# Optimization experiments

Measured on AMD Instinct MI355X. Metric: run time of the kernel, lower is better.

The kernel has to match this reference:

```python
import jax, jax.numpy as jnp
import numpy as np

N = 100000   # vertices
M = 20000    # hyperedges
NNZ = 1000000  # incidence pairs
L = 50000    # candidate links
K = 2        # vertices per link
IN, H, OUT = 256, 256, 128


def setup_inputs() -> dict:
    key = jax.random.key(0)
    ks = jax.random.split(key, 8)
    X = jax.random.normal(ks[0], (N, IN), jnp.float32)
    v_idx = jax.random.randint(ks[1], (NNZ,), 0, N, jnp.int32)
    e_idx = jax.random.randint(ks[2], (NNZ,), 0, M, jnp.int32)
    link = jax.random.randint(ks[3], (L, K), 0, N, jnp.int32)
    init = lambda k, sh, fan: jax.random.normal(k, sh, jnp.float32) / np.float32(np.sqrt(fan))
    W1 = init(ks[4], (IN, H), IN)
    b1 = jnp.zeros((H,), jnp.float32)
    W2 = init(ks[5], (H, OUT), H)
    b2 = jnp.zeros((OUT,), jnp.float32)
    fc_w = init(ks[6], (OUT, 1), OUT)
    fc_b = jnp.zeros((1,), jnp.float32)
    return dict(X=X, W1=W1, b1=b1, W2=W2, b2=b2, fc_w=fc_w, fc_b=fc_b,
                v_idx=v_idx, e_idx=e_idx, link=link)


def _segment_mean(vals, idx, num_segments):
    # mean aggregation: segment sum / segment count (count clamped to 1)
    s = jax.ops.segment_sum(vals, idx, num_segments=num_segments)
    c = jax.ops.segment_sum(jnp.ones((idx.shape[0], 1), vals.dtype), idx,
                            num_segments=num_segments)
    return s / jnp.maximum(c, 1.0)


def _hgnn_conv(X, W, b, v_idx, e_idx):
    # theta -> v2e mean -> e2v mean -> ReLU (dropout = identity in eval)
    Xt = X @ W + b                              # [N, d_out]
    Y = _segment_mean(Xt[v_idx], e_idx, M)      # [M, d_out] hyperedge feats
    Xv = _segment_mean(Y[e_idx], v_idx, N)      # [N, d_out] back to vertices
    return jax.nn.relu(Xv)


def reference(X, W1, b1, W2, b2, fc_w, fc_b, v_idx, e_idx, link):
    h1 = _hgnn_conv(X, W1, b1, v_idx, e_idx)    # extra .relu() in encode is idempotent
    h2 = _hgnn_conv(h1, W2, b2, v_idx, e_idx)   # [N, OUT]
    # per-link mean of member vertex embeddings (vectorized gather-mean)
    ex = h2[link].mean(axis=1)                  # [L, OUT]
    return jax.nn.sigmoid(ex @ fc_w + fc_b)     # [L, 1]
```

## Files before the change

kernel.cpp:

```cpp
#include <hip/hip_runtime.h>
#include <cstdint>
#include <cstddef>

#define IN_DIM  256
#define H_DIM   256
#define OUT_DIM 128
#define MEDGES  20000

typedef unsigned short u16;
typedef unsigned int   u32;
typedef short bf16x8 __attribute__((ext_vector_type(8)));
typedef float f32x4  __attribute__((ext_vector_type(4)));

__device__ __forceinline__ float bf2f(u16 u) {
    u32 x = ((u32)u) << 16;
    float f;
    __builtin_memcpy(&f, &x, 4);
    return f;
}
__device__ __forceinline__ u16 f2bf(float f) {
    u32 x;
    __builtin_memcpy(&x, &f, 4);
    u32 r = x + 0x7fffu + ((x >> 16) & 1u);
    return (u16)(r >> 16);
}

__global__ void cvt_all(const float4* __restrict__ X,  ushort4* __restrict__ Xb,  int nX,
                        const float4* __restrict__ W1, ushort4* __restrict__ W1b, int nW1,
                        const float4* __restrict__ W2, ushort4* __restrict__ W2b, int nW2)
{
    int i = blockIdx.x * blockDim.x + threadIdx.x;
    const float4* s; ushort4* d; int k;
    if (i < nX)                  { s = X;  d = Xb;  k = i; }
    else if (i < nX + nW1)       { s = W1; d = W1b; k = i - nX; }
    else if (i < nX + nW1 + nW2) { s = W2; d = W2b; k = i - nX - nW1; }
    else return;
    float4 v = s[k];
    ushort4 o;
    o.x = f2bf(v.x); o.y = f2bf(v.y); o.z = f2bf(v.z); o.w = f2bf(v.w);
    d[k] = o;
}

__global__ void hist_rank_split(const int* __restrict__ e_idx, const int* __restrict__ v_idx,
                                int* __restrict__ cnt_e, int* __restrict__ cnt_v,
                                int* __restrict__ rank_e, int* __restrict__ rank_v, int nnz)
{
    int i = blockIdx.x * blockDim.x + threadIdx.x;
    if (i < nnz) {
        rank_e[i] = atomicAdd(&cnt_e[e_idx[i]], 1);
    } else if (i < 2 * nnz) {
        int j = i - nnz;
        rank_v[j] = atomicAdd(&cnt_v[v_idx[j]], 1);
    }
}

#define SCAN_B 1024
__global__ void scan_block_both(const int* __restrict__ cnt_e, int* __restrict__ e_off,
                                const int* __restrict__ cnt_v, int* __restrict__ v_off,
                                int* __restrict__ bsums, int m, int n, int nbE)
{
    __shared__ int s[SCAN_B];
    const int* in; int* out; int* bs; int nn; int blk;
    if ((int)blockIdx.x < nbE) { in = cnt_e; out = e_off; bs = bsums;      nn = m; blk = blockIdx.x; }
    else                       { in = cnt_v; out = v_off; bs = bsums + 64; nn = n; blk = blockIdx.x - nbE; }
    int gid = blk * SCAN_B + threadIdx.x;
    int x = (gid < nn) ? in[gid] : 0;
    s[threadIdx.x] = x;
    __syncthreads();
    for (int off = 1; off < SCAN_B; off <<= 1) {
        int v = (threadIdx.x >= off) ? s[threadIdx.x - off] : 0;
        __syncthreads();
        s[threadIdx.x] += v;
        __syncthreads();
    }
    if (gid < nn) out[gid] = s[threadIdx.x] - x;
    if (threadIdx.x == SCAN_B - 1) bs[blk] = s[SCAN_B - 1];
}

__global__ void scan_top_both(int* __restrict__ bsums, int nbE, int nbV,
                              int* __restrict__ e_off, int* __restrict__ v_off,
                              int m, int n, int nnz)
{
    int t = threadIdx.x;
    if (t == 0) {
        int run = 0;
        for (int i = 0; i < nbE; ++i) { int v = bsums[i]; bsums[i] = run; run += v; }
        e_off[m] = nnz;
    } else if (t == 1) {
        int run = 0;
        for (int i = 0; i < nbV; ++i) { int v = bsums[64 + i]; bsums[64 + i] = run; run += v; }
        v_off[n] = nnz;
    }
}

__global__ void scan_add_both(int* __restrict__ e_off, int* __restrict__ v_off,
                              const int* __restrict__ bsums, int m, int n, int nbE)
{
    int* out; const int* bs; int nn; int blk;
    if ((int)blockIdx.x < nbE) { out = e_off; bs = bsums;      nn = m; blk = blockIdx.x; }
    else                       { out = v_off; bs = bsums + 64; nn = n; blk = blockIdx.x - nbE; }
    int gid = blk * SCAN_B + threadIdx.x;
    if (gid < nn) out[gid] += bs[blk];
}

__global__ void scatter_split(const int* __restrict__ e_idx, const int* __restrict__ v_idx,
                              const int* __restrict__ e_off, const int* __restrict__ v_off,
                              const int* __restrict__ rank_e, const int* __restrict__ rank_v,
                              int* __restrict__ e_list, int* __restrict__ v_list, int nnz)
{
    int i = blockIdx.x * blockDim.x + threadIdx.x;
    if (i < nnz) {
        int e = e_idx[i];
        e_list[e_off[e] + rank_e[i]] = v_idx[i];
    } else if (i < 2 * nnz) {
        int j = i - nnz;
        int v = v_idx[j];
        v_list[v_off[v] + rank_v[j]] = e_idx[j];
    }
}

__global__ void seg_mean_w4(const ushort4* __restrict__ src, ushort4* __restrict__ dst,
                            const int* __restrict__ off, const int* __restrict__ lst,
                            int nseg, int do_relu)
{
    int wid  = (blockIdx.x * blockDim.x + threadIdx.x) >> 6;
    int lane = threadIdx.x & 63;
    if (wid >= nseg) return;
    int beg = __builtin_amdgcn_readfirstlane(off[wid]);
    int end = __builtin_amdgcn_readfirstlane(off[wid + 1]);
    float ax = 0.f, ay = 0.f, az = 0.f, aw = 0.f;
    int j = beg;
    for (; j + 3 < end; j += 4) {
        int i0 = lst[j], i1 = lst[j + 1], i2 = lst[j + 2], i3 = lst[j + 3];
        ushort4 a = src[(size_t)i0 * 64 + lane];
        ushort4 b = src[(size_t)i1 * 64 + lane];
        ushort4 c = src[(size_t)i2 * 64 + lane];
        ushort4 d = src[(size_t)i3 * 64 + lane];
        ax += bf2f(a.x) + bf2f(b.x) + bf2f(c.x) + bf2f(d.x);
        ay += bf2f(a.y) + bf2f(b.y) + bf2f(c.y) + bf2f(d.y);
        az += bf2f(a.z) + bf2f(b.z) + bf2f(c.z) + bf2f(d.z);
        aw += bf2f(a.w) + bf2f(b.w) + bf2f(c.w) + bf2f(d.w);
    }
    for (; j < end; ++j) {
        ushort4 a = src[(size_t)lst[j] * 64 + lane];
        ax += bf2f(a.x); ay += bf2f(a.y); az += bf2f(a.z); aw += bf2f(a.w);
    }
    int cnt = end - beg;
    float inv = (cnt > 0) ? 1.f / (float)cnt : 0.f;
    ax *= inv; ay *= inv; az *= inv; aw *= inv;
    if (do_relu) {
        ax = fmaxf(ax, 0.f); ay = fmaxf(ay, 0.f);
        az = fmaxf(az, 0.f); aw = fmaxf(aw, 0.f);
    }
    ushort4 o;
    o.x = f2bf(ax); o.y = f2bf(ay); o.z = f2bf(az); o.w = f2bf(aw);
    dst[(size_t)wid * 64 + lane] = o;
}

__global__ void seg_mean_w2(const ushort2* __restrict__ src, ushort2* __restrict__ dst,
                            const int* __restrict__ off, const int* __restrict__ lst,
                            int nseg, int do_relu)
{
    int wid  = (blockIdx.x * blockDim.x + threadIdx.x) >> 6;
    int lane = threadIdx.x & 63;
    if (wid >= nseg) return;
    int beg = __builtin_amdgcn_readfirstlane(off[wid]);
    int end = __builtin_amdgcn_readfirstlane(off[wid + 1]);
    float ax = 0.f, ay = 0.f;
    int j = beg;
    for (; j + 3 < end; j += 4) {
        int i0 = lst[j], i1 = lst[j + 1], i2 = lst[j + 2], i3 = lst[j + 3];
        ushort2 a = src[(size_t)i0 * 64 + lane];
        ushort2 b = src[(size_t)i1 * 64 + lane];
        ushort2 c = src[(size_t)i2 * 64 + lane];
        ushort2 d = src[(size_t)i3 * 64 + lane];
        ax += bf2f(a.x) + bf2f(b.x) + bf2f(c.x) + bf2f(d.x);
        ay += bf2f(a.y) + bf2f(b.y) + bf2f(c.y) + bf2f(d.y);
    }
    for (; j < end; ++j) {
        ushort2 a = src[(size_t)lst[j] * 64 + lane];
        ax += bf2f(a.x); ay += bf2f(a.y);
    }
    int cnt = end - beg;
    float inv = (cnt > 0) ? 1.f / (float)cnt : 0.f;
    ax *= inv; ay *= inv;
    if (do_relu) { ax = fmaxf(ax, 0.f); ay = fmaxf(ay, 0.f); }
    ushort2 o;
    o.x = f2bf(ax); o.y = f2bf(ay);
    dst[(size_t)wid * 64 + lane] = o;
}

#define GSTRIDE 40
__global__ __launch_bounds__(256) void gemm_mfma_bf16(const u16* __restrict__ A,
                                                      const u16* __restrict__ W,
                                                      const float* __restrict__ bias,
                                                      u16* __restrict__ C,
                                                      int R, int K, int Cc)
{
    __shared__ __align__(16) u16 As[64 * GSTRIDE];
    __shared__ __align__(16) u16 Bs[64 * GSTRIDE];

    int tid  = threadIdx.x;
    int wave = tid >> 6;
    int lane = tid & 63;
    int quad = lane >> 4;
    int l16  = lane & 15;

    int row0 = blockIdx.y * 64;
    int col0 = blockIdx.x * 64;

    f32x4 acc[4] = {};

    int ar   = tid >> 2;
    int aseg = tid & 3;
    int bk   = tid >> 3;
    int bn   = tid & 7;

    for (int k0 = 0; k0 < K; k0 += 32) {
        bf16x8 av = {};
        int gr = row0 + ar;
        if (gr < R) av = *(const bf16x8*)&A[(size_t)gr * K + k0 + 8 * aseg];
        *(bf16x8*)&As[ar * GSTRIDE + 8 * aseg] = av;
        bf16x8 wv = *(const bf16x8*)&W[(size_t)(k0 + bk) * Cc + col0 + 8 * bn];
#pragma unroll
        for (int j = 0; j < 8; ++j)
            Bs[(8 * bn + j) * GSTRIDE + bk] = ((const u16*)&wv)[j];
        __syncthreads();

        bf16x8 af = *(const bf16x8*)&As[(16 * wave + l16) * GSTRIDE + 8 * quad];
#pragma unroll
        for (int nt = 0; nt < 4; ++nt) {
            bf16x8 bfv = *(const bf16x8*)&Bs[(16 * nt + l16) * GSTRIDE + 8 * quad];
            acc[nt] = __builtin_amdgcn_mfma_f32_16x16x32_bf16(af, bfv, acc[nt], 0, 0, 0);
        }
        __syncthreads();
    }

#pragma unroll
    for (int nt = 0; nt < 4; ++nt) {
        int col = col0 + 16 * nt + l16;
        float bv = bias[col];
#pragma unroll
        for (int r = 0; r < 4; ++r) {
            int grow = row0 + 16 * wave + 4 * quad + r;
            if (grow < R) C[(size_t)grow * Cc + col] = f2bf(acc[nt][r] + bv);
        }
    }
}

__global__ void link_head(const ushort2* __restrict__ h2, const int* __restrict__ link,
                          const float* __restrict__ fc_w, const float* __restrict__ fc_b,
                          float* __restrict__ out, int L)
{
    int gtid = blockIdx.x * blockDim.x + threadIdx.x;
    int wid  = gtid >> 6;
    int lane = threadIdx.x & 63;
    if (wid >= L) return;
    const int Dh = OUT_DIM / 2;
    int a = link[2 * wid + 0];
    int b = link[2 * wid + 1];
    ushort2 ra = h2[(size_t)a * Dh + lane];
    ushort2 rb = h2[(size_t)b * Dh + lane];
    float2 w = *(const float2*)&fc_w[2 * lane];
    float acc = 0.5f * ((bf2f(ra.x) + bf2f(rb.x)) * w.x + (bf2f(ra.y) + bf2f(rb.y)) * w.y);
#pragma unroll
    for (int off = 32; off; off >>= 1) acc += __shfl_xor(acc, off, 64);
    if (lane == 0) out[wid] = 1.f / (1.f + expf(-(acc + fc_b[0])));
}


static inline size_t align_up(size_t x, size_t a) { return (x + a - 1) & ~(a - 1); }

extern "C" void kernel_launch(void* const* d_in, const int* in_sizes, int n_in,
                              void* d_out, int out_size, void* d_ws, size_t ws_size,
                              hipStream_t stream)
{
    const float* X   = (const float*)d_in[0];
    const float* W1  = (const float*)d_in[1];
    const float* b1  = (const float*)d_in[2];
    const float* W2  = (const float*)d_in[3];
    const float* b2  = (const float*)d_in[4];
    const float* fcw = (const float*)d_in[5];
    const float* fcb = (const float*)d_in[6];
    const int* v_idx = (const int*)d_in[7];
    const int* e_idx = (const int*)d_in[8];
    const int* link  = (const int*)d_in[9];
    float* out = (float*)d_out;

    const int NNZ = in_sizes[7];
    const int N   = in_sizes[0] / IN_DIM;
    const int L   = in_sizes[9] / 2;
    const int M   = MEDGES;
    const int Mpad = (int)align_up(M, 64);

    char* p = (char*)d_ws;
    auto carve = [&](size_t bytes) -> void* {
        void* r = (void*)p;
        p += align_up(bytes, 256);
        return r;
    };
    u16*  Xb    = (u16*)carve((size_t)N * IN_DIM * 2);
    u16*  h1b   = (u16*)carve((size_t)N * H_DIM * 2);
    u16*  Aggb  = (u16*)carve((size_t)M * H_DIM * 2);
    u16*  Yb    = (u16*)carve((size_t)M * H_DIM * 2);
    u16*  W1b   = (u16*)carve((size_t)IN_DIM * H_DIM * 2);
    u16*  W2b   = (u16*)carve((size_t)H_DIM * OUT_DIM * 2);
    int*  e_off = (int*)carve((size_t)(M + 1) * 4);
    int*  v_off = (int*)carve((size_t)(N + 1) * 4);
    int*  cnt_e = (int*)carve((size_t)(Mpad + N) * 4);
    int*  cnt_v = cnt_e + Mpad;
    int*  rank_e= (int*)carve((size_t)NNZ * 4);
    int*  rank_v= (int*)carve((size_t)NNZ * 4);
    int*  e_lst = (int*)carve((size_t)NNZ * 4);
    int*  v_lst = (int*)carve((size_t)NNZ * 4);
    int*  bsums = (int*)carve(1024);

    (void)hipMemsetAsync(cnt_e, 0, (size_t)(Mpad + N) * 4, stream);

    const int tb = 256;

    int nX  = N * IN_DIM / 4;
    int nW1 = IN_DIM * H_DIM / 4;
    int nW2 = H_DIM * OUT_DIM / 4;
    cvt_all<<<(nX + nW1 + nW2 + tb - 1) / tb, tb, 0, stream>>>(
        (const float4*)X, (ushort4*)Xb, nX,
        (const float4*)W1, (ushort4*)W1b, nW1,
        (const float4*)W2, (ushort4*)W2b, nW2);

    hist_rank_split<<<(2 * NNZ + tb - 1) / tb, tb, 0, stream>>>(e_idx, v_idx, cnt_e, cnt_v,
                                                                rank_e, rank_v, NNZ);

    int nbE = (M + SCAN_B - 1) / SCAN_B;
    int nbV = (N + SCAN_B - 1) / SCAN_B;
    scan_block_both<<<nbE + nbV, SCAN_B, 0, stream>>>(cnt_e, e_off, cnt_v, v_off, bsums, M, N, nbE);
    scan_top_both<<<1, 64, 0, stream>>>(bsums, nbE, nbV, e_off, v_off, M, N, NNZ);
    scan_add_both<<<nbE + nbV, SCAN_B, 0, stream>>>(e_off, v_off, bsums, M, N, nbE);

    scatter_split<<<(2 * NNZ + tb - 1) / tb, tb, 0, stream>>>(e_idx, v_idx, e_off, v_off,
                                                              rank_e, rank_v, e_lst, v_lst, NNZ);

    seg_mean_w4<<<((size_t)M * 64 + tb - 1) / tb, tb, 0, stream>>>(
        (const ushort4*)Xb, (ushort4*)Aggb, e_off, e_lst, M, 0);
    gemm_mfma_bf16<<<dim3(H_DIM / 64, (M + 63) / 64), 256, 0, stream>>>(Aggb, W1b, b1, Yb, M, IN_DIM, H_DIM);
    seg_mean_w4<<<((size_t)N * 64 + tb - 1) / tb, tb, 0, stream>>>(
        (const ushort4*)Yb, (ushort4*)h1b, v_off, v_lst, N, 1);

    seg_mean_w4<<<((size_t)M * 64 + tb - 1) / tb, tb, 0, stream>>>(
        (const ushort4*)h1b, (ushort4*)Aggb, e_off, e_lst, M, 0);
    gemm_mfma_bf16<<<dim3(OUT_DIM / 64, (M + 63) / 64), 256, 0, stream>>>(Aggb, W2b, b2, Yb, M, H_DIM, OUT_DIM);
    seg_mean_w2<<<((size_t)N * 64 + tb - 1) / tb, tb, 0, stream>>>(
        (const ushort2*)Yb, (ushort2*)Xb, v_off, v_lst, N, 1);

    link_head<<<((size_t)L * 64 + tb - 1) / tb, tb, 0, stream>>>(
        (const ushort2*)Xb, link, fcw, fcb, out, L);
}
```

Before: 577.5 us.

## Replicate histogram counters per XCD to reduce cross-die atomic contention

The CSR-building histogram now keeps a separate counter array for each of the eight XCDs, chosen by reading the hardware XCC id, so atomics stay inside a die's local L2. Each rank is tagged in its top bits with the replica it came from. The scan sums the replicas and writes a per-replica exclusive base, and the scatter uses that base to place each entry. The cost is an 8x larger memset and more scan traffic, and the counter arrays borrow the h1b buffer as scratch space.

```diff
diff --git a/kernel.cpp b/kernel.cpp
--- a/kernel.cpp
+++ b/kernel.cpp
@@ -23,6 +23,12 @@
     __builtin_memcpy(&x, &f, 4);
     u32 r = x + 0x7fffu + ((x >> 16) & 1u);
     return (u16)(r >> 16);
+}
+
+__device__ __forceinline__ int xcc_id() {
+    int x;
+    asm volatile("s_getreg_b32 %0, hwreg(HW_REG_XCC_ID)" : "=s"(x));
+    return x & 7;
 }
 
 __global__ void cvt_all(const float4* __restrict__ X,  ushort4* __restrict__ Xb,  int nX,
@@ -41,30 +47,42 @@
     d[k] = o;
 }
 
-__global__ void hist_rank_split(const int* __restrict__ e_idx, const int* __restrict__ v_idx,
-                                int* __restrict__ cnt_e, int* __restrict__ cnt_v,
-                                int* __restrict__ rank_e, int* __restrict__ rank_v, int nnz)
-{
+__global__ void hist_rank_xcd(const int* __restrict__ e_idx, const int* __restrict__ v_idx,
+                              int* __restrict__ cnt_rep,
+                              u32* __restrict__ rank_e, u32* __restrict__ rank_v,
+                              int nnz, int seg, int mpad)
+{
+    int r = xcc_id();
+    int* my = cnt_rep + (size_t)r * seg;
+    u32 tag = (u32)r << 28;
     int i = blockIdx.x * blockDim.x + threadIdx.x;
     if (i < nnz) {
-        rank_e[i] = atomicAdd(&cnt_e[e_idx[i]], 1);
+        u32 old = (u32)atomicAdd(&my[e_idx[i]], 1);
+        rank_e[i] = old | tag;
     } else if (i < 2 * nnz) {
         int j = i - nnz;
-        rank_v[j] = atomicAdd(&cnt_v[v_idx[j]], 1);
+        u32 old = (u32)atomicAdd(&my[mpad + v_idx[j]], 1);
+        rank_v[j] = old | tag;
     }
 }
 
 #define SCAN_B 1024
-__global__ void scan_block_both(const int* __restrict__ cnt_e, int* __restrict__ e_off,
-                                const int* __restrict__ cnt_v, int* __restrict__ v_off,
-                                int* __restrict__ bsums, int m, int n, int nbE)
+__global__ void scan_block_both(int* __restrict__ cnt_rep,
+                                int* __restrict__ e_off, int* __restrict__ v_off,
+                                int* __restrict__ bsums, int m, int n, int nbE,
+                                int seg, int mpad)
 {
     __shared__ int s[SCAN_B];
-    const int* in; int* out; int* bs; int nn; int blk;
-    if ((int)blockIdx.x < nbE) { in = cnt_e; out = e_off; bs = bsums;      nn = m; blk = blockIdx.x; }
-    else                       { in = cnt_v; out = v_off; bs = bsums + 64; nn = n; blk = blockIdx.x - nbE; }
+    int* out; int* bs; int nn; int blk; int boff;
+    if ((int)blockIdx.x < nbE) { out = e_off; bs = bsums;      nn = m; blk = blockIdx.x;       boff = 0; }
+    else                       { out = v_off; bs = bsums + 64; nn = n; blk = blockIdx.x - nbE; boff = mpad; }
     int gid = blk * SCAN_B + threadIdx.x;
-    int x = (gid < nn) ? in[gid] : 0;
+    int c[8];
+    int x = 0;
+    if (gid < nn) {
+#pragma unroll
+        for (int r = 0; r < 8; ++r) { c[r] = cnt_rep[(size_t)r * seg + boff + gid]; x += c[r]; }
+    }
     s[threadIdx.x] = x;
     __syncthreads();
     for (int off = 1; off < SCAN_B; off <<= 1) {
@@ -73,7 +91,17 @@
         s[threadIdx.x] += v;
         __syncthreads();
     }
-    if (gid < nn) out[gid] = s[threadIdx.x] - x;
+    if (gid < nn) {
+        int ex = s[threadIdx.x] - x;
+        out[gid] = ex;
+        int run = ex;
+#pragma unroll
+        for (int r = 0; r < 8; ++r) {
+            int cc = c[r];
+            cnt_rep[(size_t)r * seg + boff + gid] = run;
+            run += cc;
+        }
+    }
     if (threadIdx.x == SCAN_B - 1) bs[blk] = s[SCAN_B - 1];
 }
 
@@ -94,28 +122,39 @@
 }
 
 __global__ void scan_add_both(int* __restrict__ e_off, int* __restrict__ v_off,
-                              const int* __restrict__ bsums, int m, int n, int nbE)
-{
-    int* out; const int* bs; int nn; int blk;
-    if ((int)blockIdx.x < nbE) { out = e_off; bs = bsums;      nn = m; blk = blockIdx.x; }
-    else                       { out = v_off; bs = bsums + 64; nn = n; blk = blockIdx.x - nbE; }
+                              int* __restrict__ cnt_rep, const int* __restrict__ bsums,
+                              int m, int n, int nbE, int seg, int mpad)
+{
+    int* out; const int* bs; int nn; int blk; int boff;
+    if ((int)blockIdx.x < nbE) { out = e_off; bs = bsums;      nn = m; blk = blockIdx.x;       boff = 0; }
+    else                       { out = v_off; bs = bsums + 64; nn = n; blk = blockIdx.x - nbE; boff = mpad; }
     int gid = blk * SCAN_B + threadIdx.x;
-    if (gid < nn) out[gid] += bs[blk];
+    if (gid < nn) {
+        int add = bs[blk];
+        out[gid] += add;
+#pragma unroll
+        for (int r = 0; r < 8; ++r) cnt_rep[(size_t)r * seg + boff + gid] += add;
+    }
 }
 
 __global__ void scatter_split(const int* __restrict__ e_idx, const int* __restrict__ v_idx,
-                              const int* __restrict__ e_off, const int* __restrict__ v_off,
-                              const int* __restrict__ rank_e, const int* __restrict__ rank_v,
-                              int* __restrict__ e_list, int* __restrict__ v_list, int nnz)
+                              const int* __restrict__ cnt_rep,
+                              const u32* __restrict__ rank_e, const u32* __restrict__ rank_v,
+                              int* __restrict__ e_list, int* __restrict__ v_list,
+                              int nnz, int seg, int mpad)
 {
     int i = blockIdx.x * blockDim.x + threadIdx.x;
     if (i < nnz) {
+        u32 pr = rank_e[i];
+        int r = (int)(pr >> 28);
         int e = e_idx[i];
-        e_list[e_off[e] + rank_e[i]] = v_idx[i];
+        e_list[cnt_rep[(size_t)r * seg + e] + (int)(pr & 0x0FFFFFFFu)] = v_idx[i];
     } else if (i < 2 * nnz) {
         int j = i - nnz;
+        u32 pr = rank_v[j];
+        int r = (int)(pr >> 28);
         int v = v_idx[j];
-        v_list[v_off[v] + rank_v[j]] = e_idx[j];
+        v_list[cnt_rep[(size_t)r * seg + mpad + v] + (int)(pr & 0x0FFFFFFFu)] = e_idx[j];
     }
 }
 
@@ -292,6 +331,7 @@
     const int L   = in_sizes[9] / 2;
     const int M   = MEDGES;
     const int Mpad = (int)align_up(M, 64);
+    const int SEG  = Mpad + N;
 
     char* p = (char*)d_ws;
     auto carve = [&](size_t bytes) -> void* {
@@ -307,15 +347,15 @@
     u16*  W2b   = (u16*)carve((size_t)H_DIM * OUT_DIM * 2);
     int*  e_off = (int*)carve((size_t)(M + 1) * 4);
     int*  v_off = (int*)carve((size_t)(N + 1) * 4);
-    int*  cnt_e = (int*)carve((size_t)(Mpad + N) * 4);
-    int*  cnt_v = cnt_e + Mpad;
     int*  rank_e= (int*)carve((size_t)NNZ * 4);
     int*  rank_v= (int*)carve((size_t)NNZ * 4);
     int*  e_lst = (int*)carve((size_t)NNZ * 4);
     int*  v_lst = (int*)carve((size_t)NNZ * 4);
     int*  bsums = (int*)carve(1024);
 
-    (void)hipMemsetAsync(cnt_e, 0, (size_t)(Mpad + N) * 4, stream);
+    int* cnt_rep = (int*)h1b;
+
+    (void)hipMemsetAsync(cnt_rep, 0, (size_t)8 * SEG * 4, stream);
 
     const int tb = 256;
 
@@ -327,17 +367,17 @@
         (const float4*)W1, (ushort4*)W1b, nW1,
         (const float4*)W2, (ushort4*)W2b, nW2);
 
-    hist_rank_split<<<(2 * NNZ + tb - 1) / tb, tb, 0, stream>>>(e_idx, v_idx, cnt_e, cnt_v,
-                                                                rank_e, rank_v, NNZ);
+    hist_rank_xcd<<<(2 * NNZ + tb - 1) / tb, tb, 0, stream>>>(
+        e_idx, v_idx, cnt_rep, (u32*)rank_e, (u32*)rank_v, NNZ, SEG, Mpad);
 
     int nbE = (M + SCAN_B - 1) / SCAN_B;
     int nbV = (N + SCAN_B - 1) / SCAN_B;
-    scan_block_both<<<nbE + nbV, SCAN_B, 0, stream>>>(cnt_e, e_off, cnt_v, v_off, bsums, M, N, nbE);
+    scan_block_both<<<nbE + nbV, SCAN_B, 0, stream>>>(cnt_rep, e_off, v_off, bsums, M, N, nbE, SEG, Mpad);
     scan_top_both<<<1, 64, 0, stream>>>(bsums, nbE, nbV, e_off, v_off, M, N, NNZ);
-    scan_add_both<<<nbE + nbV, SCAN_B, 0, stream>>>(e_off, v_off, bsums, M, N, nbE);
-
-    scatter_split<<<(2 * NNZ + tb - 1) / tb, tb, 0, stream>>>(e_idx, v_idx, e_off, v_off,
-                                                              rank_e, rank_v, e_lst, v_lst, NNZ);
+    scan_add_both<<<nbE + nbV, SCAN_B, 0, stream>>>(e_off, v_off, cnt_rep, bsums, M, N, nbE, SEG, Mpad);
+
+    scatter_split<<<(2 * NNZ + tb - 1) / tb, tb, 0, stream>>>(
+        e_idx, v_idx, cnt_rep, (const u32*)rank_e, (const u32*)rank_v, e_lst, v_lst, NNZ, SEG, Mpad);
 
     seg_mean_w4<<<((size_t)M * 64 + tb - 1) / tb, tb, 0, stream>>>(
         (const ushort4*)Xb, (ushort4*)Aggb, e_off, e_lst, M, 0);
```

Measured after the change: 574.9 us. About the same (-0.4%).

## Replace global-atomic CSR build with per-block LDS histograms and local scatter

Applied to the files above, without the earlier changes.

Builds the CSR incidence lists with per-block shared-memory histograms packed as 16-bit counters, instead of global atomics and stored per-element rank arrays. A column-wise prefix over per-block count rows gives each block its base offsets, and the scatter pass reuses LDS atomics to assign slots. This removes the global atomic contention, the memset and the two NNZ-sized rank arrays. In exchange it adds a strided per-column pass over 384 count rows in the scan kernel, and the vertex path makes four passes over its index chunk. The count matrices reuse the h1b buffer as scratch.

```diff
diff --git a/kernel.cpp b/kernel.cpp
--- a/kernel.cpp
+++ b/kernel.cpp
@@ -6,6 +6,12 @@
 #define H_DIM   256
 #define OUT_DIM 128
 #define MEDGES  20000
+
+#define B_E 256
+#define B_V 128
+#define QN  25600
+#define QW  (QN / 2)
+#define CT  1024
 
 typedef unsigned short u16;
 typedef unsigned int   u32;
@@ -41,30 +47,72 @@
     d[k] = o;
 }
 
-__global__ void hist_rank_split(const int* __restrict__ e_idx, const int* __restrict__ v_idx,
-                                int* __restrict__ cnt_e, int* __restrict__ cnt_v,
-                                int* __restrict__ rank_e, int* __restrict__ rank_v, int nnz)
-{
-    int i = blockIdx.x * blockDim.x + threadIdx.x;
-    if (i < nnz) {
-        rank_e[i] = atomicAdd(&cnt_e[e_idx[i]], 1);
-    } else if (i < 2 * nnz) {
-        int j = i - nnz;
-        rank_v[j] = atomicAdd(&cnt_v[v_idx[j]], 1);
+__global__ __launch_bounds__(1024) void count_lds(const int* __restrict__ e_idx,
+                                                  const int* __restrict__ v_idx,
+                                                  u16* __restrict__ counts_e,
+                                                  u16* __restrict__ counts_v,
+                                                  int nnz, int m, int n)
+{
+    __shared__ u32 hist[QW];
+    int t = threadIdx.x;
+    if ((int)blockIdx.x < B_E) {
+        int r = blockIdx.x;
+        int chunk = (nnz + B_E - 1) / B_E;
+        int beg = r * chunk, end = min(nnz, beg + chunk);
+        int ew = (m + 1) >> 1;
+        for (int w = t; w < ew; w += CT) hist[w] = 0;
+        __syncthreads();
+        for (int i = beg + t; i < end; i += CT) {
+            int e = e_idx[i];
+            atomicAdd(&hist[e >> 1], 1u << ((e & 1) * 16));
+        }
+        __syncthreads();
+        u16* row = counts_e + (size_t)r * m;
+        for (int b = t; b < m; b += CT)
+            row[b] = (u16)(hist[b >> 1] >> ((b & 1) * 16));
+    } else {
+        int r = blockIdx.x - B_E;
+        int chunk = (nnz + B_V - 1) / B_V;
+        int beg = r * chunk, end = min(nnz, beg + chunk);
+        u16* row = counts_v + (size_t)r * n;
+        for (int q = 0; q < 4; ++q) {
+            int qb = q * QN;
+            for (int w = t; w < QW; w += CT) hist[w] = 0;
+            __syncthreads();
+            for (int i = beg + t; i < end; i += CT) {
+                unsigned d = (unsigned)(v_idx[i] - qb);
+                if (d < (unsigned)QN)
+                    atomicAdd(&hist[d >> 1], 1u << ((d & 1) * 16));
+            }
+            __syncthreads();
+            for (int l = t; l < QN && qb + l < n; l += CT)
+                row[qb + l] = (u16)(hist[l >> 1] >> ((l & 1) * 16));
+            __syncthreads();
+        }
     }
 }
 
 #define SCAN_B 1024
-__global__ void scan_block_both(const int* __restrict__ cnt_e, int* __restrict__ e_off,
-                                const int* __restrict__ cnt_v, int* __restrict__ v_off,
+__global__ void scan_block_both(u16* __restrict__ counts_e, u16* __restrict__ counts_v,
+                                int* __restrict__ e_off, int* __restrict__ v_off,
                                 int* __restrict__ bsums, int m, int n, int nbE)
 {
     __shared__ int s[SCAN_B];
-    const int* in; int* out; int* bs; int nn; int blk;
-    if ((int)blockIdx.x < nbE) { in = cnt_e; out = e_off; bs = bsums;      nn = m; blk = blockIdx.x; }
-    else                       { in = cnt_v; out = v_off; bs = bsums + 64; nn = n; blk = blockIdx.x - nbE; }
+    u16* mat; int rows; int* out; int* bs; int nn; int blk;
+    if ((int)blockIdx.x < nbE) { mat = counts_e; rows = B_E; out = e_off; bs = bsums;      nn = m; blk = blockIdx.x; }
+    else                       { mat = counts_v; rows = B_V; out = v_off; bs = bsums + 64; nn = n; blk = blockIdx.x - nbE; }
     int gid = blk * SCAN_B + threadIdx.x;
-    int x = (gid < nn) ? in[gid] : 0;
+    int x = 0;
+    if (gid < nn) {
+        u32 acc = 0;
+        for (int r = 0; r < rows; ++r) {
+            size_t off = (size_t)r * nn + gid;
+            u16 c = mat[off];
+            mat[off] = (u16)acc;
+            acc += c;
+        }
+        x = (int)acc;
+    }
     s[threadIdx.x] = x;
     __syncthreads();
     for (int off = 1; off < SCAN_B; off <<= 1) {
@@ -103,19 +151,56 @@
     if (gid < nn) out[gid] += bs[blk];
 }
 
-__global__ void scatter_split(const int* __restrict__ e_idx, const int* __restrict__ v_idx,
-                              const int* __restrict__ e_off, const int* __restrict__ v_off,
-                              const int* __restrict__ rank_e, const int* __restrict__ rank_v,
-                              int* __restrict__ e_list, int* __restrict__ v_list, int nnz)
-{
-    int i = blockIdx.x * blockDim.x + threadIdx.x;
-    if (i < nnz) {
-        int e = e_idx[i];
-        e_list[e_off[e] + rank_e[i]] = v_idx[i];
-    } else if (i < 2 * nnz) {
-        int j = i - nnz;
-        int v = v_idx[j];
-        v_list[v_off[v] + rank_v[j]] = e_idx[j];
+__global__ __launch_bounds__(1024) void scatter_lds(const int* __restrict__ e_idx,
+                                                    const int* __restrict__ v_idx,
+                                                    const u16* __restrict__ counts_e,
+                                                    const u16* __restrict__ counts_v,
+                                                    const int* __restrict__ e_off,
+                                                    const int* __restrict__ v_off,
+                                                    int* __restrict__ e_list,
+                                                    int* __restrict__ v_list,
+                                                    int nnz, int m, int n)
+{
+    __shared__ u32 cur[QW];
+    int t = threadIdx.x;
+    if ((int)blockIdx.x < B_E) {
+        int r = blockIdx.x;
+        int chunk = (nnz + B_E - 1) / B_E;
+        int beg = r * chunk, end = min(nnz, beg + chunk);
+        const u32* base = (const u32*)(counts_e + (size_t)r * m);
+        int ew = (m + 1) >> 1;
+        for (int w = t; w < ew; w += CT) cur[w] = base[w];
+        __syncthreads();
+        for (int i = beg + t; i < end; i += CT) {
+            int e = e_idx[i];
+            int sh = (e & 1) * 16;
+            u32 old = atomicAdd(&cur[e >> 1], 1u << sh);
+            int rel = (int)((old >> sh) & 0xffffu);
+            e_list[e_off[e] + rel] = v_idx[i];
+        }
+    } else {
+        int r = blockIdx.x - B_E;
+        int chunk = (nnz + B_V - 1) / B_V;
+        int beg = r * chunk, end = min(nnz, beg + chunk);
+        const u16* row = counts_v + (size_t)r * n;
+        for (int q = 0; q < 4; ++q) {
+            int qb = q * QN;
+            const u32* base = (const u32*)(row + qb);
+            int nw = min(QW, (n - qb + 1) >> 1);
+            for (int w = t; w < nw; w += CT) cur[w] = base[w];
+            __syncthreads();
+            for (int i = beg + t; i < end; i += CT) {
+                int v = v_idx[i];
+                unsigned d = (unsigned)(v - qb);
+                if (d < (unsigned)QN) {
+                    int sh = (d & 1) * 16;
+                    u32 old = atomicAdd(&cur[d >> 1], 1u << sh);
+                    int rel = (int)((old >> sh) & 0xffffu);
+                    v_list[v_off[v] + rel] = e_idx[i];
+                }
+            }
+            __syncthreads();
+        }
     }
 }
 
@@ -291,7 +376,6 @@
     const int N   = in_sizes[0] / IN_DIM;
     const int L   = in_sizes[9] / 2;
     const int M   = MEDGES;
-    const int Mpad = (int)align_up(M, 64);
 
     char* p = (char*)d_ws;
     auto carve = [&](size_t bytes) -> void* {
@@ -307,15 +391,12 @@
     u16*  W2b   = (u16*)carve((size_t)H_DIM * OUT_DIM * 2);
     int*  e_off = (int*)carve((size_t)(M + 1) * 4);
     int*  v_off = (int*)carve((size_t)(N + 1) * 4);
-    int*  cnt_e = (int*)carve((size_t)(Mpad + N) * 4);
-    int*  cnt_v = cnt_e + Mpad;
-    int*  rank_e= (int*)carve((size_t)NNZ * 4);
-    int*  rank_v= (int*)carve((size_t)NNZ * 4);
     int*  e_lst = (int*)carve((size_t)NNZ * 4);
     int*  v_lst = (int*)carve((size_t)NNZ * 4);
     int*  bsums = (int*)carve(1024);
 
-    (void)hipMemsetAsync(cnt_e, 0, (size_t)(Mpad + N) * 4, stream);
+    u16* counts_e = (u16*)h1b;
+    u16* counts_v = (u16*)((char*)h1b + (size_t)B_E * M * 2);
 
     const int tb = 256;
 
@@ -327,17 +408,17 @@
         (const float4*)W1, (ushort4*)W1b, nW1,
         (const float4*)W2, (ushort4*)W2b, nW2);
 
-    hist_rank_split<<<(2 * NNZ + tb - 1) / tb, tb, 0, stream>>>(e_idx, v_idx, cnt_e, cnt_v,
-                                                                rank_e, rank_v, NNZ);
+    count_lds<<<B_E + B_V, CT, 0, stream>>>(e_idx, v_idx, counts_e, counts_v, NNZ, M, N);
 
     int nbE = (M + SCAN_B - 1) / SCAN_B;
     int nbV = (N + SCAN_B - 1) / SCAN_B;
-    scan_block_both<<<nbE + nbV, SCAN_B, 0, stream>>>(cnt_e, e_off, cnt_v, v_off, bsums, M, N, nbE);
+    scan_block_both<<<nbE + nbV, SCAN_B, 0, stream>>>(counts_e, counts_v, e_off, v_off,
+                                                      bsums, M, N, nbE);
     scan_top_both<<<1, 64, 0, stream>>>(bsums, nbE, nbV, e_off, v_off, M, N, NNZ);
     scan_add_both<<<nbE + nbV, SCAN_B, 0, stream>>>(e_off, v_off, bsums, M, N, nbE);
 
-    scatter_split<<<(2 * NNZ + tb - 1) / tb, tb, 0, stream>>>(e_idx, v_idx, e_off, v_off,
-                                                              rank_e, rank_v, e_lst, v_lst, NNZ);
+    scatter_lds<<<B_E + B_V, CT, 0, stream>>>(e_idx, v_idx, counts_e, counts_v,
+                                              e_off, v_off, e_lst, v_lst, NNZ, M, N);
 
     seg_mean_w4<<<((size_t)M * 64 + tb - 1) / tb, tb, 0, stream>>>(
         (const ushort4*)Xb, (ushort4*)Aggb, e_off, e_lst, M, 0);
```

After: 596.3 us. 1.03x slower.
